# Kernel optimization log

Measured on AMD Instinct MI355X. Metric: run time of the kernel, lower is better.

The kernel has to match this reference:

```python
import jax, jax.numpy as jnp
import numpy as np

D = 256
H = 4
DH = D // H
DFF = 1024
EPS = 1e-5


def _split_heads(x):
    B, L, _ = x.shape
    return x.reshape(B, L, H, DH).transpose(0, 2, 1, 3)  # [B,H,L,dh]


def _merge_heads(o):
    B, h, L, dh = o.shape
    return o.transpose(0, 2, 1, 3).reshape(B, L, h * dh)


def _attention(Q, K, V, M):
    # Q,K,V: [B,H,Lq/Lk,dh]; M: [B,Lq,Lk] or [B,1,Lk]
    A = jnp.einsum('bhqd,bhkd->bhqk', Q, K) / (DH ** 0.5)
    A = jnp.where(M[:, None] == 0, -jnp.inf, A)
    A = jax.nn.softmax(A, axis=-1)
    return jnp.einsum('bhqk,bhkd->bhqd', A, V)


def _layernorm(x, g, b):
    mu = jnp.mean(x, axis=-1, keepdims=True)
    var = jnp.mean(jnp.square(x - mu), axis=-1, keepdims=True)
    return (x - mu) * jax.lax.rsqrt(var + EPS) * g + b


def setup_inputs() -> dict:
    key = jax.random.key(0)
    ks = jax.random.split(key, 14)
    B, T, S = 16, 1024, 1024
    s = 1.0 / (D ** 0.5)
    inp = {
        'X_target': jax.random.normal(ks[0], (B, T, D), jnp.float32),
        'outputMask': jnp.ones((B, T), jnp.float32),
        'X_encoder': jax.random.normal(ks[1], (B, S, D), jnp.float32),
        'inputMask': jnp.ones((B, S), jnp.float32),
        'Wq1': jax.random.normal(ks[2], (D, D), jnp.float32) * s,
        'Wk1': jax.random.normal(ks[3], (D, D), jnp.float32) * s,
        'Wv1': jax.random.normal(ks[4], (D, D), jnp.float32) * s,
        'Wo1': jax.random.normal(ks[5], (D, D), jnp.float32) * s,
        'Wq2': jax.random.normal(ks[6], (D, D), jnp.float32) * s,
        'Wk2': jax.random.normal(ks[7], (D, D), jnp.float32) * s,
        'Wv2': jax.random.normal(ks[8], (D, D), jnp.float32) * s,
        'Wo2': jax.random.normal(ks[9], (D, D), jnp.float32) * s,
        'W1': jax.random.normal(ks[10], (DFF, D), jnp.float32) * s,
        'W2': jax.random.normal(ks[11], (D, DFF), jnp.float32) * (1.0 / (DFF ** 0.5)),
        'g1': jnp.ones((D,), jnp.float32), 'b1': jnp.zeros((D,), jnp.float32),
        'g2': jnp.ones((D,), jnp.float32), 'b2': jnp.zeros((D,), jnp.float32),
        'g3': jnp.ones((D,), jnp.float32), 'b3': jnp.zeros((D,), jnp.float32),
    }
    return inp


def reference(X_target, outputMask, X_encoder, inputMask,
              Wq1, Wk1, Wv1, Wo1, Wq2, Wk2, Wv2, Wo2,
              W1, W2, g1, b1, g2, b2, g3, b3):
    T = X_target.shape[1]
    # combined causal * padding mask (intended tril of ones)
    tril = jnp.tril(jnp.ones((T, T), X_target.dtype))
    M_self = outputMask[:, None, :] * tril  # [B,T,T]
    M_cross = inputMask[:, None, :]         # [B,1,S]

    # masked self-attention (Linear: x @ W.T)
    Q = _split_heads(X_target @ Wq1.T)
    K = _split_heads(X_target @ Wk1.T)
    V = _split_heads(X_target @ Wv1.T)
    O = _merge_heads(_attention(Q, K, V, M_self)) @ Wo1.T
    X = X_target + _layernorm(O, g1, b1)  # AddNorm (dropout eval=identity)

    # cross-attention; note: output proj is O @ Wo2 (no transpose) in source
    Q = _split_heads(X @ Wq2.T)
    K = _split_heads(X_encoder @ Wk2.T)
    V = _split_heads(X_encoder @ Wv2.T)
    O = _merge_heads(_attention(Q, K, V, M_cross)) @ Wo2
    X = X + _layernorm(O, g2, b2)

    # FFN with ReLU after both linears (as in source)
    F = jax.nn.relu(jax.nn.relu(X @ W1.T) @ W2.T)
    X = X + _layernorm(F, g3, b3)
    return X
```

## Files before the change

kernel.cpp:

```cpp
#include <hip/hip_runtime.h>
#include <math.h>

#define D_ 256
#define H_ 4
#define DH_ 64
#define NKT_ 16
#define TPB_BITS 10

typedef __attribute__((ext_vector_type(8))) short bf16x8;
typedef __attribute__((ext_vector_type(4))) short short4v;
typedef __attribute__((ext_vector_type(4))) float f32x4;

__device__ __forceinline__ short f2bf(float x) {
  union { float f; unsigned u; } c; c.f = x;
  unsigned r = (c.u + 0x7fffu + ((c.u >> 16) & 1u)) >> 16;
  return (short)r;
}
__device__ __forceinline__ float bf2f(short s) {
  union { unsigned u; float f; } c; c.u = ((unsigned)(unsigned short)s) << 16;
  return c.f;
}
__device__ __forceinline__ unsigned cvtpk(float lo, float hi) {
  unsigned r;
  asm("v_cvt_pk_bf16_f32 %0, %1, %2" : "=v"(r) : "v"(lo), "v"(hi));
  return r;
}
#if __has_builtin(__builtin_amdgcn_exp2f)
#define EXP2F(x) __builtin_amdgcn_exp2f(x)
#else
#define EXP2F(x) __expf(0.6931471805599453f * (x))
#endif

__device__ __forceinline__ void gl_lds16(const void* g, void* lds) {
  __builtin_amdgcn_global_load_lds((const __attribute__((address_space(1))) void*)g,
                                   (__attribute__((address_space(3))) void*)lds,
                                   16, 0, 0);
}

__global__ __launch_bounds__(256) void mask_bias(const float* __restrict__ m0,
                                                 const float* __restrict__ m1,
                                                 float* __restrict__ o0,
                                                 float* __restrict__ o1, int n) {
  int i = blockIdx.x * 256 + threadIdx.x;
  if (i < n) {
    o0[i] = (m0[i] != 0.f) ? 0.f : -1e30f;
    o1[i] = (m1[i] != 0.f) ? 0.f : -1e30f;
  }
}

template<int BN, bool ABF16, bool TRANSB, bool RELU, bool CBF16>
__global__ __launch_bounds__(256) void gemm_mfma(
    const void* __restrict__ A0, const void* __restrict__ A1, const void* __restrict__ A2,
    const float* __restrict__ B0, const float* __restrict__ B1, const float* __restrict__ B2,
    void* __restrict__ C0, void* __restrict__ C1, void* __restrict__ C2,
    int N, int K, int M, int vtrans_z, int ktile_z) {
  __shared__ short Al[2][128][72];
  __shared__ short Bl[2][BN][72];
  const int tid = threadIdx.x;
  const int w   = tid >> 6;
  const int l   = tid & 63;
  const int bn  = blockIdx.x * 128;
  const int bm  = blockIdx.y * BN;
  const int z   = blockIdx.z;
  const void*  Av = (z == 0) ? A0 : ((z == 1) ? A1 : A2);
  const float* B  = (z == 0) ? B0 : ((z == 1) ? B1 : B2);
  void*        Cv = (z == 0) ? C0 : ((z == 1) ? C1 : C2);
  constexpr int NI = BN / 32;
  const int wm = (w >> 1) * 64;
  const int wn = (w & 1) * (BN / 2);
  const int fr = l & 15;
  const int fg = l >> 4;

  f32x4 acc[4][NI];
  #pragma unroll
  for (int mi = 0; mi < 4; ++mi)
    #pragma unroll
    for (int ni = 0; ni < NI; ++ni) acc[mi][ni] = (f32x4){0.f, 0.f, 0.f, 0.f};

  const int sr = tid >> 1;
  const int sc = (tid & 1) * 32;
  constexpr int BRF = (BN == 128) ? 8 : 4;
  const int brT = (BN == 128) ? (tid >> 1) : (tid >> 2);
  const int bcT = (BN == 128) ? ((tid & 1) * 32) : ((tid & 3) * 16);

  float4 arf[8]; bf16x8 arb[4]; float4 brf[8];

  auto loadA = [&](int k0) {
    if (ABF16) {
      const short* arow = (const short*)Av + (size_t)(bn + sr) * K + k0 + sc;
      #pragma unroll
      for (int i = 0; i < 4; ++i) arb[i] = *(const bf16x8*)&arow[i * 8];
    } else {
      const float* arow = (const float*)Av + (size_t)(bn + sr) * K + k0 + sc;
      #pragma unroll
      for (int i = 0; i < 8; ++i) arf[i] = *(const float4*)&arow[i * 4];
    }
  };
  auto loadB = [&](int k0) {
    if (TRANSB) {
      const float* brow = B + (size_t)(bm + brT) * K + k0 + bcT;
      #pragma unroll
      for (int i = 0; i < BRF; ++i) brf[i] = *(const float4*)&brow[i * 4];
    } else {
      #pragma unroll
      for (int i = 0; i < BRF; ++i) {
        int idx = tid + i * 256;
        int kk = (BN == 128) ? (idx >> 5) : (idx >> 4);
        int c4 = (BN == 128) ? ((idx & 31) * 4) : ((idx & 15) * 4);
        brf[i] = *(const float4*)&B[(size_t)(k0 + kk) * M + bm + c4];
      }
    }
  };
  auto store = [&](int buf) {
    if (ABF16) {
      #pragma unroll
      for (int i = 0; i < 4; ++i) *(bf16x8*)&Al[buf][sr][sc + i * 8] = arb[i];
    } else {
      #pragma unroll
      for (int i = 0; i < 8; ++i) {
        float4 v = arf[i];
        short4v s; s[0] = f2bf(v.x); s[1] = f2bf(v.y); s[2] = f2bf(v.z); s[3] = f2bf(v.w);
        *(short4v*)&Al[buf][sr][sc + i * 4] = s;
      }
    }
    if (TRANSB) {
      #pragma unroll
      for (int i = 0; i < BRF; ++i) {
        float4 v = brf[i];
        short4v s; s[0] = f2bf(v.x); s[1] = f2bf(v.y); s[2] = f2bf(v.z); s[3] = f2bf(v.w);
        *(short4v*)&Bl[buf][brT][bcT + i * 4] = s;
      }
    } else {
      #pragma unroll
      for (int i = 0; i < BRF; ++i) {
        int idx = tid + i * 256;
        int kk = (BN == 128) ? (idx >> 5) : (idx >> 4);
        int c4 = (BN == 128) ? ((idx & 31) * 4) : ((idx & 15) * 4);
        float4 v = brf[i];
        Bl[buf][c4 + 0][kk] = f2bf(v.x);
        Bl[buf][c4 + 1][kk] = f2bf(v.y);
        Bl[buf][c4 + 2][kk] = f2bf(v.z);
        Bl[buf][c4 + 3][kk] = f2bf(v.w);
      }
    }
  };

  loadA(0); loadB(0); store(0);
  __syncthreads();
  const int nk = K >> 6;
  for (int s = 0; s < nk; ++s) {
    const int cur = s & 1;
    if (s + 1 < nk) { loadA((s + 1) << 6); loadB((s + 1) << 6); }
    #pragma unroll
    for (int kh = 0; kh < 2; ++kh) {
      bf16x8 af[4], bfr[NI];
      #pragma unroll
      for (int mi = 0; mi < 4; ++mi)
        af[mi] = *(bf16x8*)&Al[cur][wm + mi * 16 + fr][kh * 32 + fg * 8];
      #pragma unroll
      for (int ni = 0; ni < NI; ++ni)
        bfr[ni] = *(bf16x8*)&Bl[cur][wn + ni * 16 + fr][kh * 32 + fg * 8];
      #pragma unroll
      for (int mi = 0; mi < 4; ++mi)
        #pragma unroll
        for (int ni = 0; ni < NI; ++ni)
          acc[mi][ni] = __builtin_amdgcn_mfma_f32_16x16x32_bf16(af[mi], bfr[ni], acc[mi][ni], 0, 0, 0);
    }
    if (s + 1 < nk) store(cur ^ 1);
    __syncthreads();
  }

  bool done = false;
  if constexpr (BN == 128) {
    if (z == vtrans_z) {
      done = true;
      #pragma unroll
      for (int mi = 0; mi < 4; ++mi) {
        int nbase = bn + wm + mi * 16 + fg * 4;
        int b_  = nbase >> TPB_BITS;
        int key = nbase & ((1 << TPB_BITS) - 1);
        int kt  = key >> 6, kin = key & 63;
        #pragma unroll
        for (int ni = 0; ni < 4; ++ni) {
          int col = bm + wn + ni * 16 + fr;
          int h_ = col >> 6, dh = col & 63;
          short4v s;
          #pragma unroll
          for (int reg = 0; reg < 4; ++reg) s[reg] = f2bf(acc[mi][ni][reg]);
          size_t off = ((((size_t)(b_ * H_ + h_) * NKT_) + kt) << 12)
                     + dh * 64 + (((kin >> 3) ^ (dh & 7)) << 3) + (kin & 7);
          *(short4v*)&((short*)Cv)[off] = s;
        }
      }
    } else if (z == ktile_z) {
      done = true;
      #pragma unroll
      for (int mi = 0; mi < 4; ++mi) {
        #pragma unroll
        for (int reg = 0; reg < 4; ++reg) {
          int tok = bn + wm + mi * 16 + fg * 4 + reg;
          int b_  = tok >> TPB_BITS;
          int key = tok & ((1 << TPB_BITS) - 1);
          int kt  = key >> 6, kin = key & 63;
          int fk  = (kin & 3) | (((kin >> 3) & 1) << 2);
          size_t tb = ((((size_t)(b_ * H_) * NKT_) + kt) << 12) + kin * 64;
          #pragma unroll
          for (int ni = 0; ni < 4; ++ni) {
            int col = bm + wn + ni * 16 + fr;
            int h_ = col >> 6, dh = col & 63;
            size_t off = tb + (((size_t)h_ * NKT_) << 12)
                       + (((dh >> 3) ^ fk) << 3) + (dh & 7);
            ((short*)Cv)[off] = f2bf(acc[mi][ni][reg]);
          }
        }
      }
    }
  }
  if (!done) {
    #pragma unroll
    for (int mi = 0; mi < 4; ++mi) {
      #pragma unroll
      for (int reg = 0; reg < 4; ++reg) {
        size_t rowbase = (size_t)(bn + wm + mi * 16 + fg * 4 + reg) * M + bm + wn;
        #pragma unroll
        for (int ni = 0; ni < NI; ++ni) {
          float v = acc[mi][ni][reg];
          if (RELU) v = fmaxf(v, 0.f);
          if (CBF16) ((short*)Cv)[rowbase + ni * 16 + fr] = f2bf(v);
          else       ((float*)Cv)[rowbase + ni * 16 + fr] = v;
        }
      }
    }
  }
}

template<bool CAUSAL>
__global__ __launch_bounds__(256) void attn_mfma(const short* __restrict__ Q,
                                                 const short* __restrict__ KT,
                                                 const short* __restrict__ VT,
                                                 const float* __restrict__ bias,
                                                 short* __restrict__ O,
                                                 int T, int Lk) {
  __shared__ short Kl[2][64][64];
  __shared__ short Vl[2][64][64];
  const int tid = threadIdx.x;
  const int l   = tid & 63;
  const int w   = tid >> 6;
  const int bh  = blockIdx.x;
  const int b   = bh >> 2;
  const int h   = bh & 3;
  const int r   = l & 15;
  const int g   = l >> 4;
  const float SCL2E = 0.125f * 1.4426950408889634f;

  const short* Ktile = KT + (((size_t)bh * (Lk >> 6)) << 12);
  const short* Vtile = VT + (((size_t)bh * (Lk >> 6)) << 12);
  const float* brow  = bias + (size_t)b * Lk;

  const int qt  = CAUSAL ? ((T >> 6) - 1 - (int)blockIdx.y) : (int)blockIdx.y;
  const int nkt = CAUSAL ? (qt + 1) : (Lk >> 6);

  bf16x8 qf[2];
  {
    const short* qrow = Q + ((size_t)(b * T + qt * 64 + w * 16 + r)) * D_ + h * DH_;
    qf[0] = *(const bf16x8*)&qrow[g * 8];
    qf[1] = *(const bf16x8*)&qrow[32 + g * 8];
  }

  float m = -1e30f, ls = 0.f;
  f32x4 acc[4];
  #pragma unroll
  for (int dt = 0; dt < 4; ++dt) acc[dt] = (f32x4){0.f, 0.f, 0.f, 0.f};

  auto stage = [&](int kt, int bb) {
    const short* ks = Ktile + ((size_t)kt << 12) + w * 1024 + (size_t)l * 8;
    const short* vs = Vtile + ((size_t)kt << 12) + w * 1024 + (size_t)l * 8;
    char* kd = (char*)&Kl[bb][0][0] + w * 2048;
    char* vd = (char*)&Vl[bb][0][0] + w * 2048;
    gl_lds16(ks,       kd);
    gl_lds16(ks + 512, kd + 1024);
    gl_lds16(vs,       vd);
    gl_lds16(vs + 512, vd + 1024);
  };

  stage(0, 0);
  __syncthreads();

  const int rx = r & 7;
  const int rowp = 8 * (r >> 2) + (r & 3);
  for (int kt = 0; kt < nkt; ++kt) {
    const int buf = kt & 1;
    if (kt + 1 < nkt) stage(kt + 1, buf ^ 1);

    const char* kb = (const char*)&Kl[buf][0][0];
    const char* vb = (const char*)&Vl[buf][0][0];

    f32x4 sfr[4];
    #pragma unroll
    for (int st = 0; st < 4; ++st) sfr[st] = (f32x4){0.f, 0.f, 0.f, 0.f};
    __builtin_amdgcn_s_setprio(1);
    #pragma unroll
    for (int st = 0; st < 4; ++st) {
      const int rowk = 32 * (st >> 1) + 4 * (st & 1) + rowp;
      #pragma unroll
      for (int kh = 0; kh < 2; ++kh) {
        bf16x8 kf = *(const bf16x8*)(kb + rowk * 128 + (((kh * 4 + g) ^ rx) << 4));
        sfr[st] = __builtin_amdgcn_mfma_f32_16x16x32_bf16(kf, qf[kh], sfr[st], 0, 0, 0);
      }
    }
    __builtin_amdgcn_s_setprio(0);

    float sc[4][4];
    #pragma unroll
    for (int st = 0; st < 4; ++st) {
      float4 mv = *(const float4*)&brow[kt * 64 + 32 * (st >> 1) + 4 * (st & 1) + 8 * g];
      sc[st][0] = fmaf(sfr[st][0], SCL2E, mv.x);
      sc[st][1] = fmaf(sfr[st][1], SCL2E, mv.y);
      sc[st][2] = fmaf(sfr[st][2], SCL2E, mv.z);
      sc[st][3] = fmaf(sfr[st][3], SCL2E, mv.w);
    }
    if (CAUSAL && kt == qt) {
      #pragma unroll
      for (int st = 0; st < 4; ++st)
        #pragma unroll
        for (int reg = 0; reg < 4; ++reg)
          if (32 * (st >> 1) + 4 * (st & 1) + 8 * g + reg > w * 16 + r)
            sc[st][reg] = -1e30f;
    }

    float t0 = fmaxf(fmaxf(sc[0][0], sc[0][1]), sc[0][2]);
    float t1 = fmaxf(fmaxf(sc[0][3], sc[1][0]), sc[1][1]);
    float t2 = fmaxf(fmaxf(sc[1][2], sc[1][3]), sc[2][0]);
    float t3 = fmaxf(fmaxf(sc[2][1], sc[2][2]), sc[2][3]);
    float t4 = fmaxf(fmaxf(sc[3][0], sc[3][1]), sc[3][2]);
    float tm = fmaxf(fmaxf(fmaxf(t0, t1), fmaxf(t2, t3)), fmaxf(t4, sc[3][3]));
    tm = fmaxf(tm, __shfl_xor(tm, 16));
    tm = fmaxf(tm, __shfl_xor(tm, 32));
    const int need = __any(tm - m > 8.f);
    float mnew = need ? fmaxf(m, tm) : m;
    float pe[4][4], psum = 0.f;
    #pragma unroll
    for (int st = 0; st < 4; ++st)
      #pragma unroll
      for (int reg = 0; reg < 4; ++reg) {
        pe[st][reg] = EXP2F(sc[st][reg] - mnew);
        psum += pe[st][reg];
      }
    psum += __shfl_xor(psum, 16);
    psum += __shfl_xor(psum, 32);

    union { unsigned u[4]; bf16x8 v; } pa, pb;
    pa.u[0] = cvtpk(pe[0][0], pe[0][1]);
    pa.u[1] = cvtpk(pe[0][2], pe[0][3]);
    pa.u[2] = cvtpk(pe[1][0], pe[1][1]);
    pa.u[3] = cvtpk(pe[1][2], pe[1][3]);
    pb.u[0] = cvtpk(pe[2][0], pe[2][1]);
    pb.u[1] = cvtpk(pe[2][2], pe[2][3]);
    pb.u[2] = cvtpk(pe[3][0], pe[3][1]);
    pb.u[3] = cvtpk(pe[3][2], pe[3][3]);

    if (need) {
      float alpha = EXP2F(m - mnew);
      ls = ls * alpha + psum;
      m = mnew;
      float af[4];
      #pragma unroll
      for (int reg = 0; reg < 4; ++reg) af[reg] = __shfl(alpha, g * 4 + reg);
      #pragma unroll
      for (int dt = 0; dt < 4; ++dt)
        #pragma unroll
        for (int reg = 0; reg < 4; ++reg) acc[dt][reg] *= af[reg];
    } else {
      ls += psum;
    }

    __builtin_amdgcn_s_setprio(1);
    #pragma unroll
    for (int kh = 0; kh < 2; ++kh) {
      bf16x8 pf = (kh == 0) ? pa.v : pb.v;
      #pragma unroll
      for (int dt = 0; dt < 4; ++dt) {
        bf16x8 vf = *(const bf16x8*)(vb + (dt * 16 + r) * 128 + (((kh * 4 + g) ^ rx) << 4));
        acc[dt] = __builtin_amdgcn_mfma_f32_16x16x32_bf16(pf, vf, acc[dt], 0, 0, 0);
      }
    }
    __builtin_amdgcn_s_setprio(0);

    __syncthreads();
  }

  float inv = (ls > 0.f) ? (1.f / ls) : 0.f;
  float invf[4];
  #pragma unroll
  for (int reg = 0; reg < 4; ++reg) invf[reg] = __shfl(inv, g * 4 + reg);
  #pragma unroll
  for (int reg = 0; reg < 4; ++reg) {
    short* orow = O + ((size_t)(b * T + qt * 64 + w * 16 + g * 4 + reg)) * D_ + h * DH_;
    #pragma unroll
    for (int dt = 0; dt < 4; ++dt)
      orow[dt * 16 + r] = f2bf(acc[dt][reg] * invf[reg]);
  }
}

template<bool RBF16, bool OBF16>
__global__ __launch_bounds__(256) void ln_res(const short* __restrict__ F,
                                              const void* __restrict__ Rv,
                                              const float* __restrict__ g,
                                              const float* __restrict__ bt,
                                              void* __restrict__ outv) {
  const int lane = threadIdx.x & 63;
  const int wid  = threadIdx.x >> 6;
  const size_t row  = (size_t)blockIdx.x * 4 + wid;
  const size_t base = row * 256 + (size_t)lane * 4;
  short4v fv = *(const short4v*)&F[base];
  float vx = bf2f(fv[0]), vy = bf2f(fv[1]), vz = bf2f(fv[2]), vw = bf2f(fv[3]);
  float s = vx + vy + vz + vw;
  #pragma unroll
  for (int o = 32; o >= 1; o >>= 1) s += __shfl_xor(s, o);
  float mu = s * (1.f / 256.f);
  float dx = vx - mu, dy = vy - mu, dz = vz - mu, dw = vw - mu;
  float vr = dx * dx + dy * dy + dz * dz + dw * dw;
  #pragma unroll
  for (int o = 32; o >= 1; o >>= 1) vr += __shfl_xor(vr, o);
  float rstd = rsqrtf(vr * (1.f / 256.f) + 1e-5f);
  float4 g4 = *(const float4*)&g[lane * 4];
  float4 b4 = *(const float4*)&bt[lane * 4];
  float rx, ry, rz, rw;
  if (RBF16) {
    short4v r4 = *(const short4v*)&((const short*)Rv)[base];
    rx = bf2f(r4[0]); ry = bf2f(r4[1]); rz = bf2f(r4[2]); rw = bf2f(r4[3]);
  } else {
    float4 r4 = *(const float4*)&((const float*)Rv)[base];
    rx = r4.x; ry = r4.y; rz = r4.z; rw = r4.w;
  }
  float ox = fmaf(dx * rstd, g4.x, b4.x) + rx;
  float oy = fmaf(dy * rstd, g4.y, b4.y) + ry;
  float oz = fmaf(dz * rstd, g4.z, b4.z) + rz;
  float ow = fmaf(dw * rstd, g4.w, b4.w) + rw;
  if (OBF16) {
    uint2 u; u.x = cvtpk(ox, oy); u.y = cvtpk(oz, ow);
    *(uint2*)&((short*)outv)[base] = u;
  } else {
    *(float4*)&((float*)outv)[base] = make_float4(ox, oy, oz, ow);
  }
}

extern "C" void kernel_launch(void* const* d_in, const int* in_sizes, int n_in,
                              void* d_out, int out_size, void* d_ws, size_t ws_size,
                              hipStream_t stream) {
  const float* Xt    = (const float*)d_in[0];
  const float* oMask = (const float*)d_in[1];
  const float* Xe    = (const float*)d_in[2];
  const float* iMask = (const float*)d_in[3];
  const float* Wq1   = (const float*)d_in[4];
  const float* Wk1   = (const float*)d_in[5];
  const float* Wv1   = (const float*)d_in[6];
  const float* Wo1   = (const float*)d_in[7];
  const float* Wq2   = (const float*)d_in[8];
  const float* Wk2   = (const float*)d_in[9];
  const float* Wv2   = (const float*)d_in[10];
  const float* Wo2   = (const float*)d_in[11];
  const float* W1    = (const float*)d_in[12];
  const float* W2    = (const float*)d_in[13];
  const float* g1    = (const float*)d_in[14];
  const float* b1    = (const float*)d_in[15];
  const float* g2    = (const float*)d_in[16];
  const float* b2    = (const float*)d_in[17];
  const float* g3    = (const float*)d_in[18];
  const float* b3    = (const float*)d_in[19];

  const int B = 16, T = 1024, S = 1024;
  const int NT = B * T;
  const size_t SZ = (size_t)NT * 256;

  float* ws = (float*)d_ws;
  float* s0 = ws;
  float* s1 = ws + SZ;
  float* s2 = ws + 2 * SZ;
  float* s3 = ws + 3 * SZ;
  float* s4 = ws + 4 * SZ;
  float* s5 = ws + 5 * SZ;
  short* b_s0 = (short*)s0; short* b_s1 = (short*)s1; short* b_s2 = (short*)s2;
  short* b_s3 = (short*)s3; short* b_s4 = (short*)s4; short* b_s5 = (short*)s5;
  float* biasS = s3 + 3 * (SZ / 4);
  float* biasC = biasS + B * S;

  dim3 blk(256);
  dim3 gQKV(NT / 128, 2, 3);
  dim3 gKV(NT / 128, 2, 2);
  dim3 gS64(NT / 128, 4, 1);
  dim3 gF1(NT / 128, 8, 1);
  dim3 gA(B * H_, T / 64);

  mask_bias<<<64, blk, 0, stream>>>(oMask, iMask, biasS, biasC, B * T);

  gemm_mfma<128, false, true, false, true><<<gQKV, blk, 0, stream>>>(
      Xt, Xt, Xt, Wq1, Wk1, Wv1, s0, s1, s2, NT, 256, 256, 2, 1);
  attn_mfma<true><<<gA, blk, 0, stream>>>(b_s0, b_s1, b_s2, biasS, b_s3, T, T);
  gemm_mfma<64, true, true, false, true><<<gS64, blk, 0, stream>>>(
      s3, s3, s3, Wo1, Wo1, Wo1, s0, s0, s0, NT, 256, 256, -1, -1);
  ln_res<false, true><<<NT / 4, blk, 0, stream>>>(b_s0, Xt, g1, b1, b_s4);

  gemm_mfma<64, true, true, false, true><<<gS64, blk, 0, stream>>>(
      s4, s4, s4, Wq2, Wq2, Wq2, s0, s0, s0, NT, 256, 256, -1, -1);
  gemm_mfma<128, false, true, false, true><<<gKV, blk, 0, stream>>>(
      Xe, Xe, Xe, Wk2, Wv2, Wv2, s1, s2, s2, NT, 256, 256, 1, 0);
  attn_mfma<false><<<gA, blk, 0, stream>>>(b_s0, b_s1, b_s2, biasC, b_s3, T, S);
  gemm_mfma<64, true, false, false, true><<<gS64, blk, 0, stream>>>(
      s3, s3, s3, Wo2, Wo2, Wo2, s0, s0, s0, NT, 256, 256, -1, -1);
  ln_res<true, true><<<NT / 4, blk, 0, stream>>>(b_s0, b_s4, g2, b2, b_s5);

  gemm_mfma<128, true, true, true, true><<<gF1, blk, 0, stream>>>(
      s5, s5, s5, W1, W1, W1, s0, s0, s0, NT, 256, 1024, -1, -1);
  gemm_mfma<64, true, true, true, true><<<gS64, blk, 0, stream>>>(
      s0, s0, s0, W2, W2, W2, s4, s4, s4, NT, 1024, 256, -1, -1);
  ln_res<true, false><<<NT / 4, blk, 0, stream>>>(b_s4, b_s5, g3, b3, (float*)d_out);
}
```

Baseline: 217.3 us.

## Merge cross-attn Q/KV projections, fold softmax scale into Q, skip unmasked bias tiles

```diff
diff --git a/kernel.cpp b/kernel.cpp
--- a/kernel.cpp
+++ b/kernel.cpp
@@ -6,6 +6,7 @@
 #define DH_ 64
 #define NKT_ 16
 #define TPB_BITS 10
+#define SCL2E_ 0.18033688011112042f
 
 typedef __attribute__((ext_vector_type(8))) short bf16x8;
 typedef __attribute__((ext_vector_type(4))) short short4v;
@@ -40,11 +41,24 @@
 __global__ __launch_bounds__(256) void mask_bias(const float* __restrict__ m0,
                                                  const float* __restrict__ m1,
                                                  float* __restrict__ o0,
-                                                 float* __restrict__ o1, int n) {
+                                                 float* __restrict__ o1,
+                                                 float* __restrict__ f0,
+                                                 float* __restrict__ f1, int n) {
   int i = blockIdx.x * 256 + threadIdx.x;
   if (i < n) {
     o0[i] = (m0[i] != 0.f) ? 0.f : -1e30f;
     o1[i] = (m1[i] != 0.f) ? 0.f : -1e30f;
+  }
+  if (blockIdx.x == 0) {
+    int t = threadIdx.x;
+    const float* ms = m0 + (t >> 4) * 1024 + (t & 15) * 64;
+    const float* mc = m1 + (t >> 4) * 1024 + (t & 15) * 64;
+    float fs = 0.f, fc = 0.f;
+    for (int j = 0; j < 64; ++j) {
+      if (ms[j] == 0.f) fs = 1.f;
+      if (mc[j] == 0.f) fc = 1.f;
+    }
+    f0[t] = fs; f1[t] = fc;
   }
 }
 
@@ -53,7 +67,7 @@
     const void* __restrict__ A0, const void* __restrict__ A1, const void* __restrict__ A2,
     const float* __restrict__ B0, const float* __restrict__ B1, const float* __restrict__ B2,
     void* __restrict__ C0, void* __restrict__ C1, void* __restrict__ C2,
-    int N, int K, int M, int vtrans_z, int ktile_z) {
+    int N, int K, int M, int vtrans_z, int ktile_z, int abf16_z, int qscale_z) {
   __shared__ short Al[2][128][72];
   __shared__ short Bl[2][BN][72];
   const int tid = threadIdx.x;
@@ -65,6 +79,7 @@
   const void*  Av = (z == 0) ? A0 : ((z == 1) ? A1 : A2);
   const float* B  = (z == 0) ? B0 : ((z == 1) ? B1 : B2);
   void*        Cv = (z == 0) ? C0 : ((z == 1) ? C1 : C2);
+  const bool abf = ABF16 || (z == abf16_z);
   constexpr int NI = BN / 32;
   const int wm = (w >> 1) * 64;
   const int wn = (w & 1) * (BN / 2);
@@ -86,7 +101,7 @@
   float4 arf[8]; bf16x8 arb[4]; float4 brf[8];
 
   auto loadA = [&](int k0) {
-    if (ABF16) {
+    if (abf) {
       const short* arow = (const short*)Av + (size_t)(bn + sr) * K + k0 + sc;
       #pragma unroll
       for (int i = 0; i < 4; ++i) arb[i] = *(const bf16x8*)&arow[i * 8];
@@ -112,7 +127,7 @@
     }
   };
   auto store = [&](int buf) {
-    if (ABF16) {
+    if (abf) {
       #pragma unroll
       for (int i = 0; i < 4; ++i) *(bf16x8*)&Al[buf][sr][sc + i * 8] = arb[i];
     } else {
@@ -217,6 +232,7 @@
     }
   }
   if (!done) {
+    const float cs = (z == qscale_z) ? SCL2E_ : 1.f;
     #pragma unroll
     for (int mi = 0; mi < 4; ++mi) {
       #pragma unroll
@@ -224,7 +240,7 @@
         size_t rowbase = (size_t)(bn + wm + mi * 16 + fg * 4 + reg) * M + bm + wn;
         #pragma unroll
         for (int ni = 0; ni < NI; ++ni) {
-          float v = acc[mi][ni][reg];
+          float v = acc[mi][ni][reg] * cs;
           if (RELU) v = fmaxf(v, 0.f);
           if (CBF16) ((short*)Cv)[rowbase + ni * 16 + fr] = f2bf(v);
           else       ((float*)Cv)[rowbase + ni * 16 + fr] = v;
@@ -239,6 +255,7 @@
                                                  const short* __restrict__ KT,
                                                  const short* __restrict__ VT,
                                                  const float* __restrict__ bias,
+                                                 const float* __restrict__ flags,
                                                  short* __restrict__ O,
                                                  int T, int Lk) {
   __shared__ short Kl[2][64][64];
@@ -251,11 +268,11 @@
   const int h   = bh & 3;
   const int r   = l & 15;
   const int g   = l >> 4;
-  const float SCL2E = 0.125f * 1.4426950408889634f;
 
   const short* Ktile = KT + (((size_t)bh * (Lk >> 6)) << 12);
   const short* Vtile = VT + (((size_t)bh * (Lk >> 6)) << 12);
   const float* brow  = bias + (size_t)b * Lk;
+  const float* bfl   = flags + b * NKT_;
 
   const int qt  = CAUSAL ? ((T >> 6) - 1 - (int)blockIdx.y) : (int)blockIdx.y;
   const int nkt = CAUSAL ? (qt + 1) : (Lk >> 6);
@@ -311,13 +328,20 @@
     __builtin_amdgcn_s_setprio(0);
 
     float sc[4][4];
-    #pragma unroll
-    for (int st = 0; st < 4; ++st) {
-      float4 mv = *(const float4*)&brow[kt * 64 + 32 * (st >> 1) + 4 * (st & 1) + 8 * g];
-      sc[st][0] = fmaf(sfr[st][0], SCL2E, mv.x);
-      sc[st][1] = fmaf(sfr[st][1], SCL2E, mv.y);
-      sc[st][2] = fmaf(sfr[st][2], SCL2E, mv.z);
-      sc[st][3] = fmaf(sfr[st][3], SCL2E, mv.w);
+    if (bfl[kt] != 0.f) {
+      #pragma unroll
+      for (int st = 0; st < 4; ++st) {
+        float4 mv = *(const float4*)&brow[kt * 64 + 32 * (st >> 1) + 4 * (st & 1) + 8 * g];
+        sc[st][0] = sfr[st][0] + mv.x;
+        sc[st][1] = sfr[st][1] + mv.y;
+        sc[st][2] = sfr[st][2] + mv.z;
+        sc[st][3] = sfr[st][3] + mv.w;
+      }
+    } else {
+      #pragma unroll
+      for (int st = 0; st < 4; ++st)
+        #pragma unroll
+        for (int reg = 0; reg < 4; ++reg) sc[st][reg] = sfr[st][reg];
     }
     if (CAUSAL && kt == qt) {
       #pragma unroll
@@ -484,35 +508,34 @@
   short* b_s3 = (short*)s3; short* b_s4 = (short*)s4; short* b_s5 = (short*)s5;
   float* biasS = s3 + 3 * (SZ / 4);
   float* biasC = biasS + B * S;
+  float* flagS = biasC + B * S;
+  float* flagC = flagS + B * NKT_;
 
   dim3 blk(256);
   dim3 gQKV(NT / 128, 2, 3);
-  dim3 gKV(NT / 128, 2, 2);
   dim3 gS64(NT / 128, 4, 1);
   dim3 gF1(NT / 128, 8, 1);
   dim3 gA(B * H_, T / 64);
 
-  mask_bias<<<64, blk, 0, stream>>>(oMask, iMask, biasS, biasC, B * T);
+  mask_bias<<<64, blk, 0, stream>>>(oMask, iMask, biasS, biasC, flagS, flagC, B * T);
 
   gemm_mfma<128, false, true, false, true><<<gQKV, blk, 0, stream>>>(
-      Xt, Xt, Xt, Wq1, Wk1, Wv1, s0, s1, s2, NT, 256, 256, 2, 1);
-  attn_mfma<true><<<gA, blk, 0, stream>>>(b_s0, b_s1, b_s2, biasS, b_s3, T, T);
+      Xt, Xt, Xt, Wq1, Wk1, Wv1, s0, s1, s2, NT, 256, 256, 2, 1, -1, 0);
+  attn_mfma<true><<<gA, blk, 0, stream>>>(b_s0, b_s1, b_s2, biasS, flagS, b_s3, T, T);
   gemm_mfma<64, true, true, false, true><<<gS64, blk, 0, stream>>>(
-      s3, s3, s3, Wo1, Wo1, Wo1, s0, s0, s0, NT, 256, 256, -1, -1);
+      s3, s3, s3, Wo1, Wo1, Wo1, s0, s0, s0, NT, 256, 256, -1, -1, -1, -1);
   ln_res<false, true><<<NT / 4, blk, 0, stream>>>(b_s0, Xt, g1, b1, b_s4);
 
-  gemm_mfma<64, true, true, false, true><<<gS64, blk, 0, stream>>>(
-      s4, s4, s4, Wq2, Wq2, Wq2, s0, s0, s0, NT, 256, 256, -1, -1);
-  gemm_mfma<128, false, true, false, true><<<gKV, blk, 0, stream>>>(
-      Xe, Xe, Xe, Wk2, Wv2, Wv2, s1, s2, s2, NT, 256, 256, 1, 0);
-  attn_mfma<false><<<gA, blk, 0, stream>>>(b_s0, b_s1, b_s2, biasC, b_s3, T, S);
+  gemm_mfma<128, false, true, false, true><<<gQKV, blk, 0, stream>>>(
+      s4, Xe, Xe, Wq2, Wk2, Wv2, s0, s1, s2, NT, 256, 256, 2, 1, 0, 0);
+  attn_mfma<false><<<gA, blk, 0, stream>>>(b_s0, b_s1, b_s2, biasC, flagC, b_s3, T, S);
   gemm_mfma<64, true, false, false, true><<<gS64, blk, 0, stream>>>(
-      s3, s3, s3, Wo2, Wo2, Wo2, s0, s0, s0, NT, 256, 256, -1, -1);
+      s3, s3, s3, Wo2, Wo2, Wo2, s0, s0, s0, NT, 256, 256, -1, -1, -1, -1);
   ln_res<true, true><<<NT / 4, blk, 0, stream>>>(b_s0, b_s4, g2, b2, b_s5);
 
   gemm_mfma<128, true, true, true, true><<<gF1, blk, 0, stream>>>(
-      s5, s5, s5, W1, W1, W1, s0, s0, s0, NT, 256, 1024, -1, -1);
+      s5, s5, s5, W1, W1, W1, s0, s0, s0, NT, 256, 1024, -1, -1, -1, -1);
   gemm_mfma<64, true, true, true, true><<<gS64, blk, 0, stream>>>(
-      s0, s0, s0, W2, W2, W2, s4, s4, s4, NT, 1024, 256, -1, -1);
+      s0, s0, s0, W2, W2, W2, s4, s4, s4, NT, 1024, 256, -1, -1, -1, -1);
   ln_res<true, false><<<NT / 4, blk, 0, stream>>>(b_s4, b_s5, g3, b3, (float*)d_out);
 }
```

Measured after the change: 210.3 us. 3.2% less time.
